# Kernel tuning notes

Measured on AMD Instinct MI355X. Metric: run time of the kernel, lower is better.

The kernel has to match this reference:

```python
import jax, jax.numpy as jnp
import numpy as np

NUM_HEADS = 16
HEAD_DIM = 80  # head_dim_ori; NPU pads 80->128 with zeros (math-neutral)


def _rotate_half(x):
    x1, x2 = jnp.split(x, 2, axis=-1)
    return jnp.concatenate([-x2, x1], axis=-1)


def setup_inputs() -> dict:
    key = jax.random.key(0)
    ks = jax.random.split(key, 7)
    S, E = 4096, 1280
    inv = jnp.asarray(1.0 / np.sqrt(E), jnp.float32)
    # rotary tables: proper cos/sin from angles for realism
    pos = jnp.arange(S, dtype=jnp.float32)[:, None]
    freqs = 1.0 / (10000.0 ** (jnp.arange(0, HEAD_DIM // 2, dtype=jnp.float32) / (HEAD_DIM // 2)))
    ang = pos * freqs[None, :]                      # [S, 40]
    ang = jnp.concatenate([ang, ang], axis=-1)      # [S, 80] rotate-half layout
    return {
        'hidden_states': jax.random.normal(ks[0], (S, E), jnp.float32),
        'cos': jnp.cos(ang),
        'sin': jnp.sin(ang),
        'w_qkv': jax.random.normal(ks[1], (3 * E, E), jnp.float32) * inv,
        'b_qkv': jax.random.normal(ks[2], (3 * E,), jnp.float32) * 0.02,
        'w_proj': jax.random.normal(ks[3], (E, E), jnp.float32) * inv,
        'b_proj': jax.random.normal(ks[4], (E,), jnp.float32) * 0.02,
    }


def reference(hidden_states, cos, sin, w_qkv, b_qkv, w_proj, b_proj):
    S, E = hidden_states.shape
    H, D = NUM_HEADS, HEAD_DIM
    # fused QKV linear (transposeB=True, hasBias=True) then split into 3
    qkv = hidden_states @ w_qkv.T + b_qkv          # [S, 3E]
    q, k, v = jnp.split(qkv, 3, axis=-1)
    q = q.reshape(S, H, D)
    k = k.reshape(S, H, D)
    v = v.reshape(S, H, D)
    # rotate-half RoPE (rotaryCoeff=2) on q and k
    c = cos[:, None, :]
    s = sin[:, None, :]
    q = q * c + _rotate_half(q) * s
    k = k * c + _rotate_half(k) * s
    # full bidirectional self-attention (PA_ENCODER), qkScale = 1/sqrt(head_dim_ori)
    scale = jnp.asarray(1.0 / np.sqrt(D), q.dtype)
    scores = jnp.einsum('shd,thd->hst', q, k) * scale   # [H, S, S]
    attn = jax.nn.softmax(scores, axis=-1)
    out = jnp.einsum('hst,thd->shd', attn, v).reshape(S, E)
    # output projection + residual add (atten_res_add)
    dense = out @ w_proj.T + b_proj
    return hidden_states + dense
```

## Files before the change

kernel.cpp:

```cpp
#include <hip/hip_runtime.h>
#include <hip/hip_bf16.h>


#define S_LEN 4096
#define E_DIM 1280
#define NH 16
#define HD 80
#define HDP 96

typedef __bf16 bf16x8 __attribute__((ext_vector_type(8)));
typedef float f32x4 __attribute__((ext_vector_type(4)));

__device__ __forceinline__ short f2bf(float x) {
    __hip_bfloat16 h = __float2bfloat16(x);
    return __builtin_bit_cast(short, h);
}
__device__ __forceinline__ float bf2f(short x) {
    return __bfloat162float(__builtin_bit_cast(__hip_bfloat16, x));
}
__device__ __forceinline__ bf16x8 ldb(const short* p) {
    return *reinterpret_cast<const bf16x8*>(p);
}
__device__ __forceinline__ unsigned cvt_pk_bf16(float a, float b) {
    unsigned r;
    asm("v_cvt_pk_bf16_f32 %0, %1, %2" : "=v"(r) : "v"(a), "v"(b));
    return r;
}
__device__ __forceinline__ void gload16(const void* g, void* l) {
    __builtin_amdgcn_global_load_lds(
        (const __attribute__((address_space(1))) unsigned int*)g,
        (__attribute__((address_space(3))) unsigned int*)l, 16, 0, 0);
}

__global__ __launch_bounds__(256) void cast3_k(const float* __restrict__ a, short* __restrict__ oa, int na4,
                                               const float* __restrict__ b, short* __restrict__ ob, int nb4,
                                               const float* __restrict__ c, short* __restrict__ oc, int nc4) {
    int j = blockIdx.x * 256 + threadIdx.x;
    const float* src;
    short* dst;
    if (j < na4) {
        src = a; dst = oa;
    } else {
        j -= na4;
        if (j < nb4) {
            src = b; dst = ob;
        } else {
            j -= nb4;
            if (j >= nc4) return;
            src = c; dst = oc;
        }
    }
    float4 v = *reinterpret_cast<const float4*>(&src[j * 4]);
    ushort4 o;
    o.x = (unsigned short)f2bf(v.x);
    o.y = (unsigned short)f2bf(v.y);
    o.z = (unsigned short)f2bf(v.z);
    o.w = (unsigned short)f2bf(v.w);
    *reinterpret_cast<ushort4*>(&dst[j * 4]) = o;
}

__global__ __launch_bounds__(512, 2) void gemm1_256_k(
    const short* __restrict__ A, const short* __restrict__ B, const float* __restrict__ bias,
    short* __restrict__ Qraw, short* __restrict__ Kraw, short* __restrict__ Vg) {
    const int K = E_DIM;
    __shared__ short As[2][2][8192];
    __shared__ short Bs[2][2][8192];
    int t = threadIdx.x;
    int lane = t & 63, w = t >> 6;
    int wr = w >> 2, wc = w & 3;
    int lr = lane & 15, lg = lane >> 4;
    int bid = blockIdx.x;
    int swz = (bid & 7) * 30 + (bid >> 3);
    int bm = swz / 15, bn = swz % 15;
    int mb = bm * 256, nb = bn * 256;

    int lgs = (t & 3) ^ ((t >> 3) & 3);
    const short* aS = A + (size_t)(mb + (t >> 2)) * K + lgs * 8;
    const short* bS = B + (size_t)(nb + (t >> 2)) * K + lgs * 8;
    const int rowStep = 128 * K;

    int aoff[2][4], boff[4];
#pragma unroll
    for (int mq = 0; mq < 2; mq++)
#pragma unroll
        for (int ii = 0; ii < 4; ii++) {
            int r = wr * 128 + mq * 64 + ii * 16 + lr;
            aoff[mq][ii] = r * 32 + ((lg ^ ((r >> 1) & 3)) * 8);
        }
#pragma unroll
    for (int n = 0; n < 4; n++) {
        int r = wc * 64 + n * 16 + lr;
        boff[n] = r * 32 + ((lg ^ ((r >> 1) & 3)) * 8);
    }

    f32x4 acc[8][4];
#pragma unroll
    for (int i = 0; i < 8; i++)
#pragma unroll
        for (int n = 0; n < 4; n++) acc[i][n] = (f32x4){0.f, 0.f, 0.f, 0.f};

#define STG_A(d, kh, kb2)                                              \
    {                                                                  \
        gload16(aS + (kb2) + (kh)*32, &As[d][kh][w * 512]);            \
        gload16(aS + rowStep + (kb2) + (kh)*32, &As[d][kh][4096 + w * 512]); \
    }
#define STG_B(d, kh, kb2)                                              \
    {                                                                  \
        gload16(bS + (kb2) + (kh)*32, &Bs[d][kh][w * 512]);            \
        gload16(bS + rowStep + (kb2) + (kh)*32, &Bs[d][kh][4096 + w * 512]); \
    }

    STG_A(0, 0, 0);
    STG_B(0, 0, 0);
    STG_A(0, 1, 0);
    STG_B(0, 1, 0);
    asm volatile("s_waitcnt vmcnt(4)" ::: "memory");
    __builtin_amdgcn_s_barrier();
    asm volatile("" ::: "memory");

    for (int kb = 0; kb < K; kb += 64) {
        int d = (kb >> 6) & 1;
        int kb2 = kb + 64;
        bool more = kb2 < K;
        bf16x8 af[4], bfr[4];

#pragma unroll
        for (int n = 0; n < 4; n++) bfr[n] = ldb(&Bs[d][0][boff[n]]);
#pragma unroll
        for (int ii = 0; ii < 4; ii++) af[ii] = ldb(&As[d][0][aoff[0][ii]]);
        if (more) STG_A(d ^ 1, 0, kb2);
        __builtin_amdgcn_s_barrier();
        asm volatile("s_waitcnt lgkmcnt(0)" ::: "memory");
        __builtin_amdgcn_sched_barrier(0);
        __builtin_amdgcn_s_setprio(1);
#pragma unroll
        for (int ii = 0; ii < 4; ii++)
#pragma unroll
            for (int n = 0; n < 4; n++)
                acc[ii][n] = __builtin_amdgcn_mfma_f32_16x16x32_bf16(af[ii], bfr[n], acc[ii][n], 0, 0, 0);
        __builtin_amdgcn_s_setprio(0);
        __builtin_amdgcn_s_barrier();
        asm volatile("" ::: "memory");

#pragma unroll
        for (int ii = 0; ii < 4; ii++) af[ii] = ldb(&As[d][0][aoff[1][ii]]);
        if (more) {
            STG_B(d ^ 1, 0, kb2);
            asm volatile("s_waitcnt vmcnt(4)" ::: "memory");
        } else {
            asm volatile("s_waitcnt vmcnt(0)" ::: "memory");
        }
        __builtin_amdgcn_s_barrier();
        asm volatile("s_waitcnt lgkmcnt(0)" ::: "memory");
        __builtin_amdgcn_sched_barrier(0);
        __builtin_amdgcn_s_setprio(1);
#pragma unroll
        for (int ii = 0; ii < 4; ii++)
#pragma unroll
            for (int n = 0; n < 4; n++)
                acc[4 + ii][n] = __builtin_amdgcn_mfma_f32_16x16x32_bf16(af[ii], bfr[n], acc[4 + ii][n], 0, 0, 0);
        __builtin_amdgcn_s_setprio(0);
        __builtin_amdgcn_s_barrier();
        asm volatile("" ::: "memory");

#pragma unroll
        for (int n = 0; n < 4; n++) bfr[n] = ldb(&Bs[d][1][boff[n]]);
#pragma unroll
        for (int ii = 0; ii < 4; ii++) af[ii] = ldb(&As[d][1][aoff[0][ii]]);
        if (more) STG_A(d ^ 1, 1, kb2);
        __builtin_amdgcn_s_barrier();
        asm volatile("s_waitcnt lgkmcnt(0)" ::: "memory");
        __builtin_amdgcn_sched_barrier(0);
        __builtin_amdgcn_s_setprio(1);
#pragma unroll
        for (int ii = 0; ii < 4; ii++)
#pragma unroll
            for (int n = 0; n < 4; n++)
                acc[ii][n] = __builtin_amdgcn_mfma_f32_16x16x32_bf16(af[ii], bfr[n], acc[ii][n], 0, 0, 0);
        __builtin_amdgcn_s_setprio(0);
        __builtin_amdgcn_s_barrier();
        asm volatile("" ::: "memory");

#pragma unroll
        for (int ii = 0; ii < 4; ii++) af[ii] = ldb(&As[d][1][aoff[1][ii]]);
        if (more) {
            STG_B(d ^ 1, 1, kb2);
            asm volatile("s_waitcnt vmcnt(4)" ::: "memory");
        }
        __builtin_amdgcn_s_barrier();
        asm volatile("s_waitcnt lgkmcnt(0)" ::: "memory");
        __builtin_amdgcn_sched_barrier(0);
        __builtin_amdgcn_s_setprio(1);
#pragma unroll
        for (int ii = 0; ii < 4; ii++)
#pragma unroll
            for (int n = 0; n < 4; n++)
                acc[4 + ii][n] = __builtin_amdgcn_mfma_f32_16x16x32_bf16(af[ii], bfr[n], acc[4 + ii][n], 0, 0, 0);
        __builtin_amdgcn_s_setprio(0);
        __builtin_amdgcn_s_barrier();
        asm volatile("" ::: "memory");
    }
#undef STG_A
#undef STG_B

    int part = nb / E_DIM;
    short* dst = (part == 0) ? Qraw : (part == 1) ? Kraw : Vg;
#pragma unroll
    for (int j = 0; j < 4; j++) {
        int n = nb + wc * 64 + j * 16 + lr;
        float bv = bias[n];
        int hd = n - part * E_DIM;
        int h = hd / HD, dd = hd - h * HD;
#pragma unroll
        for (int i = 0; i < 8; i++) {
#pragma unroll
            for (int r = 0; r < 4; r++) {
                int s = mb + wr * 128 + (i >> 2) * 64 + (i & 3) * 16 + lg * 4 + r;
                dst[(h * S_LEN + s) * HD + dd] = f2bf(acc[i][j][r] + bv);
            }
        }
    }
}

__global__ __launch_bounds__(256) void gemm_bt_k(
    const short* __restrict__ A, const short* __restrict__ B, const float* __restrict__ bias,
    const float* __restrict__ resid, float* __restrict__ Out) {
    const int K = E_DIM;
    __shared__ short As[2][128 * 64];
    __shared__ short Bs[2][128 * 64];
    int t = threadIdx.x;
    int lane = t & 63, w = t >> 6;
    int wr = w >> 1, wc = w & 1;
    int lr = lane & 15, lg = lane >> 4;
    int mb = blockIdx.y * 128, nb = blockIdx.x * 128;

    const short* asrc[4];
    const short* bsrc[4];
#pragma unroll
    for (int c = 0; c < 4; c++) {
        int p = c * 256 + t;
        int m = p >> 3;
        int kg = (p & 7) ^ (m & 7);
        asrc[c] = A + (size_t)(mb + m) * K + kg * 8;
        bsrc[c] = B + (size_t)(nb + m) * K + kg * 8;
    }
    int xa = lr & 7;
    int cx0 = ((0 * 4 + lg) ^ xa) * 8;
    int cx1 = ((1 * 4 + lg) ^ xa) * 8;
    int rowA[4], rowB[4];
#pragma unroll
    for (int i = 0; i < 4; i++) {
        rowA[i] = (wr * 64 + i * 16 + lr) * 64;
        rowB[i] = (wc * 64 + i * 16 + lr) * 64;
    }

    f32x4 acc[4][4];
#pragma unroll
    for (int i = 0; i < 4; i++)
#pragma unroll
        for (int j = 0; j < 4; j++) acc[i][j] = (f32x4){0.f, 0.f, 0.f, 0.f};

#define G_STAGE(buf, kb)                                             \
    {                                                                \
        _Pragma("unroll") for (int c = 0; c < 4; c++) {              \
            int ldso = c * 2048 + w * 512;                           \
            gload16(asrc[c] + (kb), &As[buf][ldso]);                 \
            gload16(bsrc[c] + (kb), &Bs[buf][ldso]);                 \
        }                                                            \
    }

    G_STAGE(0, 0);
    asm volatile("s_waitcnt vmcnt(0)" ::: "memory");
    __syncthreads();

    int buf = 0;
    for (int kb = 0; kb < K; kb += 64) {
        if (kb + 64 < K) G_STAGE(buf ^ 1, kb + 64);
        __builtin_amdgcn_s_setprio(1);
#pragma unroll
        for (int kk = 0; kk < 2; kk++) {
            int cx = kk ? cx1 : cx0;
            bf16x8 af[4], bfr[4];
#pragma unroll
            for (int i = 0; i < 4; i++) {
                af[i] = ldb(&As[buf][rowA[i] + cx]);
                bfr[i] = ldb(&Bs[buf][rowB[i] + cx]);
            }
#pragma unroll
            for (int i = 0; i < 4; i++)
#pragma unroll
                for (int j = 0; j < 4; j++)
                    acc[i][j] = __builtin_amdgcn_mfma_f32_16x16x32_bf16(af[i], bfr[j], acc[i][j], 0, 0, 0);
        }
        __builtin_amdgcn_s_setprio(0);
        __syncthreads();
        buf ^= 1;
    }
#undef G_STAGE

#pragma unroll
    for (int j = 0; j < 4; j++) {
        int n = nb + wc * 64 + j * 16 + lr;
        float bv = bias[n];
#pragma unroll
        for (int i = 0; i < 4; i++) {
#pragma unroll
            for (int r = 0; r < 4; r++) {
                int s = mb + wr * 64 + i * 16 + lg * 4 + r;
                Out[s * E_DIM + n] = acc[i][j][r] + bv + resid[s * E_DIM + n];
            }
        }
    }
}

__global__ __launch_bounds__(256) void rope_k(const short* __restrict__ Qraw,
                                              const short* __restrict__ Kraw,
                                              const float* __restrict__ cosp,
                                              const float* __restrict__ sinp,
                                              short* __restrict__ Qg, short* __restrict__ Kg) {
    int idx = blockIdx.x * 256 + threadIdx.x;
    int c = idx % 12;
    int sh = idx / 12;
    int s = sh & (S_LEN - 1);
    int base96 = sh * HDP + c * 8;
    if (c >= 10) {
        int4 z = {0, 0, 0, 0};
        *reinterpret_cast<int4*>(&Qg[base96]) = z;
        *reinterpret_cast<int4*>(&Kg[base96]) = z;
        return;
    }
    int d0 = c * 8;
    int dp = (d0 < 40) ? d0 + 40 : d0 - 40;
    float sgn = (d0 < 40) ? -1.f : 1.f;
    int base80 = sh * HD;
    float q[8], qp[8], k[8], kp[8], cs[8], sn[8];
    {
        int4 v;
        v = *reinterpret_cast<const int4*>(&Qraw[base80 + d0]);
        const short* sp = reinterpret_cast<const short*>(&v);
        for (int i = 0; i < 8; i++) q[i] = bf2f(sp[i]);
        v = *reinterpret_cast<const int4*>(&Qraw[base80 + dp]);
        for (int i = 0; i < 8; i++) qp[i] = bf2f(sp[i]);
        v = *reinterpret_cast<const int4*>(&Kraw[base80 + d0]);
        for (int i = 0; i < 8; i++) k[i] = bf2f(sp[i]);
        v = *reinterpret_cast<const int4*>(&Kraw[base80 + dp]);
        for (int i = 0; i < 8; i++) kp[i] = bf2f(sp[i]);
    }
    *reinterpret_cast<float4*>(&cs[0]) = *reinterpret_cast<const float4*>(&cosp[s * HD + d0]);
    *reinterpret_cast<float4*>(&cs[4]) = *reinterpret_cast<const float4*>(&cosp[s * HD + d0 + 4]);
    *reinterpret_cast<float4*>(&sn[0]) = *reinterpret_cast<const float4*>(&sinp[s * HD + d0]);
    *reinterpret_cast<float4*>(&sn[4]) = *reinterpret_cast<const float4*>(&sinp[s * HD + d0 + 4]);
    const float qscale = 0.16129849190f;
    short oq[8], ok[8];
#pragma unroll
    for (int i = 0; i < 8; i++) {
        oq[i] = f2bf((q[i] * cs[i] + sgn * qp[i] * sn[i]) * qscale);
        ok[i] = f2bf(k[i] * cs[i] + sgn * kp[i] * sn[i]);
    }
    *reinterpret_cast<int4*>(&Qg[base96]) = *reinterpret_cast<int4*>(oq);
    *reinterpret_cast<int4*>(&Kg[base96]) = *reinterpret_cast<int4*>(ok);
}

__global__ __launch_bounds__(256) void transpose_v_k(const short* __restrict__ Vg,
                                                     short* __restrict__ Vt) {
    __shared__ short tile[32][33];
    int h = blockIdx.z, sb = blockIdx.x * 32, db = blockIdx.y * 32;
    int t = threadIdx.x;
    for (int e = t; e < 1024; e += 256) {
        int si = e >> 5, dj = e & 31;
        int d = db + dj;
        tile[si][dj] = (d < HD) ? Vg[(h * S_LEN + sb + si) * HD + d] : (short)0;
    }
    __syncthreads();
    for (int e = t; e < 1024; e += 256) {
        int di = e >> 5, sj = e & 31;
        int d = db + di;
        if (d < HD) Vt[(h * HD + d) * S_LEN + sb + sj] = tile[sj][di];
    }
}

__global__ __launch_bounds__(512, 4) void attn_k(const short* __restrict__ Qg,
                                                 const short* __restrict__ Kg,
                                                 const short* __restrict__ Vt,
                                                 short* __restrict__ Ob) {
    __shared__ __align__(16) short smem[35072];
    short* ksb = smem;
    short* vsb = smem + 13312;
    short* psb = smem + 24832;

    int t = threadIdx.x;
    int lane = t & 63, w = t >> 6;
    int lr = lane & 15, lg = lane >> 4;
    int pairi = w >> 1, half = w & 1;
    int L = blockIdx.x;
    int h = ((L & 7) << 1) | (L >> 8);
    int qb = ((L >> 3) & 31) << 7;

    const short* kgp = Kg + (size_t)h * S_LEN * HDP;
    const short* vgp = Vt + (size_t)h * HD * S_LEN;

    bf16x8 qf[2][3];
#pragma unroll
    for (int qq = 0; qq < 2; qq++) {
        const short* qp = Qg + ((size_t)h * S_LEN + qb + pairi * 32 + qq * 16 + lr) * HDP;
#pragma unroll
        for (int kk = 0; kk < 3; kk++) qf[qq][kk] = ldb(qp + kk * 32 + lg * 8);
    }
    f32x4 o[2][5];
#pragma unroll
    for (int qq = 0; qq < 2; qq++)
#pragma unroll
        for (int nd = 0; nd < 5; nd++) o[qq][nd] = (f32x4){0.f, 0.f, 0.f, 0.f};
    f32x4 l4[2] = {(f32x4){0.f, 0.f, 0.f, 0.f}, (f32x4){0.f, 0.f, 0.f, 0.f}};

    int gk0 = t, rk0 = gk0 / 13, ok0 = gk0 % 13;
    if (ok0 == 12) ok0 = 0;
    const short* ksrc0 = kgp + rk0 * HDP + ok0 * 8;
    int gk1 = t + 512, rk1 = gk1 / 13, ok1 = gk1 % 13;
    if (ok1 == 12) ok1 = 0;
    const short* ksrc1 = kgp + rk1 * HDP + ok1 * 8;
    int gv0 = t, rv0 = gv0 / 9, ov0 = gv0 % 9;
    if (ov0 == 8) ov0 = 0;
    const short* vsrc0 = vgp + (size_t)rv0 * S_LEN + ov0 * 8;
    bool v1v = (t + 512) < 720;
    int gv1 = t + 512, rv1 = gv1 / 9, ov1 = gv1 % 9;
    if (ov1 == 8) ov1 = 0;
    const short* vsrc1 = vgp + (size_t)rv1 * S_LEN + ov1 * 8;

#define A_STAGE(buf, kb)                                                          \
    {                                                                             \
        gload16(ksrc0 + (size_t)(kb) * HDP, ksb + (buf)*6656 + w * 512);          \
        if (w < 5) gload16(ksrc1 + (size_t)(kb) * HDP, ksb + (buf)*6656 + 4096 + w * 512); \
        gload16(vsrc0 + (kb), vsb + (buf)*5760 + w * 512);                        \
        if (v1v) gload16(vsrc1 + (kb), vsb + (buf)*5760 + 4096 + w * 512);        \
    }

    A_STAGE(0, 0);
    asm volatile("s_waitcnt vmcnt(0)" ::: "memory");
    __syncthreads();

    short* ps = psb + w * 1280;
    int buf = 0;
    for (int kb = 0; kb < S_LEN; kb += 64) {
        if (kb + 64 < S_LEN) A_STAGE(buf ^ 1, kb + 64);
        const short* ks = ksb + buf * 6656;
        const short* vs = vsb + buf * 5760;

        f32x4 sc[2][2];
#pragma unroll
        for (int qq = 0; qq < 2; qq++)
#pragma unroll
            for (int n = 0; n < 2; n++) sc[qq][n] = (f32x4){0.f, 0.f, 0.f, 0.f};
        __builtin_amdgcn_s_setprio(1);
#pragma unroll
        for (int n = 0; n < 2; n++) {
#pragma unroll
            for (int kk = 0; kk < 3; kk++) {
                bf16x8 kf = ldb(&ks[(half * 32 + n * 16 + lr) * 104 + kk * 32 + lg * 8]);
                sc[0][n] = __builtin_amdgcn_mfma_f32_16x16x32_bf16(kf, qf[0][kk], sc[0][n], 0, 0, 0);
                sc[1][n] = __builtin_amdgcn_mfma_f32_16x16x32_bf16(kf, qf[1][kk], sc[1][n], 0, 0, 0);
            }
        }
        __builtin_amdgcn_s_setprio(0);

#pragma unroll
        for (int qq = 0; qq < 2; qq++) {
#pragma unroll
            for (int n = 0; n < 2; n++) {
#pragma unroll
                for (int r = 0; r < 4; r++) sc[qq][n][r] = __builtin_amdgcn_exp2f(sc[qq][n][r]);
                l4[qq] += sc[qq][n];
                uint2 pk;
                pk.x = cvt_pk_bf16(sc[qq][n][0], sc[qq][n][1]);
                pk.y = cvt_pk_bf16(sc[qq][n][2], sc[qq][n][3]);
                *reinterpret_cast<uint2*>(&ps[(qq * 16 + lr) * 40 + n * 16 + lg * 4]) = pk;
            }
        }

        bf16x8 pf0 = ldb(&ps[(0 * 16 + lr) * 40 + lg * 8]);
        bf16x8 pf1 = ldb(&ps[(1 * 16 + lr) * 40 + lg * 8]);
        __builtin_amdgcn_s_setprio(1);
#pragma unroll
        for (int nd = 0; nd < 5; nd++) {
            bf16x8 vf = ldb(&vs[(nd * 16 + lr) * 72 + half * 32 + lg * 8]);
            o[0][nd] = __builtin_amdgcn_mfma_f32_16x16x32_bf16(pf0, vf, o[0][nd], 0, 0, 0);
            o[1][nd] = __builtin_amdgcn_mfma_f32_16x16x32_bf16(pf1, vf, o[1][nd], 0, 0, 0);
        }
        __builtin_amdgcn_s_setprio(0);

        __syncthreads();
        buf ^= 1;
    }
#undef A_STAGE

    float lh[2];
#pragma unroll
    for (int qq = 0; qq < 2; qq++) {
        float l = l4[qq][0] + l4[qq][1] + l4[qq][2] + l4[qq][3];
        l += __shfl_xor(l, 16);
        l += __shfl_xor(l, 32);
        lh[qq] = l;
    }
    float* Osc = reinterpret_cast<float*>(smem);
    float* lsc = reinterpret_cast<float*>(smem) + 10240;
    if (half) {
#pragma unroll
        for (int qq = 0; qq < 2; qq++) {
#pragma unroll
            for (int nd = 0; nd < 5; nd++)
#pragma unroll
                for (int r = 0; r < 4; r++)
                    Osc[(pairi * 32 + qq * 16 + lg * 4 + r) * 80 + nd * 16 + lr] = o[qq][nd][r];
            if (lg == 0) lsc[pairi * 32 + qq * 16 + lr] = lh[qq];
        }
    }
    __syncthreads();
    if (!half) {
        float rl[2][4];
#pragma unroll
        for (int qq = 0; qq < 2; qq++) {
            float lt = lh[qq] + lsc[pairi * 32 + qq * 16 + lr];
#pragma unroll
            for (int r = 0; r < 4; r++) {
                float lf = __shfl(lt, lg * 4 + r);
                rl[qq][r] = __builtin_amdgcn_rcpf(lf);
            }
        }
#pragma unroll
        for (int qq = 0; qq < 2; qq++)
#pragma unroll
            for (int nd = 0; nd < 5; nd++)
#pragma unroll
                for (int r = 0; r < 4; r++) {
                    int s = qb + pairi * 32 + qq * 16 + lg * 4 + r;
                    float val = o[qq][nd][r] + Osc[(pairi * 32 + qq * 16 + lg * 4 + r) * 80 + nd * 16 + lr];
                    Ob[s * E_DIM + h * HD + nd * 16 + lr] = f2bf(val * rl[qq][r]);
                }
    }
}

extern "C" void kernel_launch(void* const* d_in, const int* in_sizes, int n_in,
                              void* d_out, int out_size, void* d_ws, size_t ws_size,
                              hipStream_t stream) {
    const float* hidden = (const float*)d_in[0];
    const float* cosp = (const float*)d_in[1];
    const float* sinp = (const float*)d_in[2];
    const float* wqkv = (const float*)d_in[3];
    const float* bqkv = (const float*)d_in[4];
    const float* wproj = (const float*)d_in[5];
    const float* bproj = (const float*)d_in[6];
    float* out = (float*)d_out;

    char* p = (char*)d_ws;
    short* Xb = (short*)p;      p += (size_t)S_LEN * E_DIM * 2;
    short* Wqkvb = (short*)p;   p += (size_t)3 * E_DIM * E_DIM * 2;
    short* Wprojb = (short*)p;  p += (size_t)E_DIM * E_DIM * 2;
    short* Qraw = (short*)p;    p += (size_t)NH * S_LEN * HD * 2;
    short* Kraw = (short*)p;    p += (size_t)NH * S_LEN * HD * 2;
    short* Vg = (short*)p;      p += (size_t)NH * S_LEN * HD * 2;
    short* Qg = (short*)p;      p += (size_t)NH * S_LEN * HDP * 2;
    short* Kg = (short*)p;      p += (size_t)NH * S_LEN * HDP * 2;
    short* Vt = (short*)p;      p += (size_t)NH * HD * S_LEN * 2;
    short* Ob = Xb;

    const int na4 = S_LEN * E_DIM / 4;
    const int nb4 = 3 * E_DIM * E_DIM / 4;
    const int nc4 = E_DIM * E_DIM / 4;
    cast3_k<<<(na4 + nb4 + nc4 + 255) / 256, 256, 0, stream>>>(
        hidden, Xb, na4, wqkv, Wqkvb, nb4, wproj, Wprojb, nc4);

    gemm1_256_k<<<dim3(240), 512, 0, stream>>>(Xb, Wqkvb, bqkv, Qraw, Kraw, Vg);

    rope_k<<<NH * S_LEN * 12 / 256, 256, 0, stream>>>(Qraw, Kraw, cosp, sinp, Qg, Kg);

    transpose_v_k<<<dim3(S_LEN / 32, 3, NH), 256, 0, stream>>>(Vg, Vt);

    attn_k<<<dim3(512), 512, 0, stream>>>(Qg, Kg, Vt, Ob);

    gemm_bt_k<<<dim3(E_DIM / 128, S_LEN / 128), 256, 0, stream>>>(
        Ob, Wprojb, bproj, hidden, out);
}
```

Before: 206.5 us.

## Keep P in registers for PV MFMA and store QKV row-major

After: 197.3 us. 4.4% less time.

```diff
diff --git a/kernel.cpp b/kernel.cpp
--- a/kernel.cpp
+++ b/kernel.cpp
@@ -205,18 +205,18 @@
 
     int part = nb / E_DIM;
     short* dst = (part == 0) ? Qraw : (part == 1) ? Kraw : Vg;
+    int nloc = nb - part * E_DIM;
 #pragma unroll
     for (int j = 0; j < 4; j++) {
-        int n = nb + wc * 64 + j * 16 + lr;
-        float bv = bias[n];
-        int hd = n - part * E_DIM;
-        int h = hd / HD, dd = hd - h * HD;
+        int cn = wc * 64 + j * 16 + lr;
+        float bv = bias[nb + cn];
+        int col = nloc + cn;
 #pragma unroll
         for (int i = 0; i < 8; i++) {
 #pragma unroll
             for (int r = 0; r < 4; r++) {
                 int s = mb + wr * 128 + (i >> 2) * 64 + (i & 3) * 16 + lg * 4 + r;
-                dst[(h * S_LEN + s) * HD + dd] = f2bf(acc[i][j][r] + bv);
+                dst[(size_t)s * E_DIM + col] = f2bf(acc[i][j][r] + bv);
             }
         }
     }
@@ -320,9 +320,9 @@
                                               short* __restrict__ Qg, short* __restrict__ Kg) {
     int idx = blockIdx.x * 256 + threadIdx.x;
     int c = idx % 12;
-    int sh = idx / 12;
-    int s = sh & (S_LEN - 1);
-    int base96 = sh * HDP + c * 8;
+    int hh = (idx / 12) & 15;
+    int s = idx / 192;
+    int base96 = ((hh * S_LEN + s)) * HDP + c * 8;
     if (c >= 10) {
         int4 z = {0, 0, 0, 0};
         *reinterpret_cast<int4*>(&Qg[base96]) = z;
@@ -332,7 +332,7 @@
     int d0 = c * 8;
     int dp = (d0 < 40) ? d0 + 40 : d0 - 40;
     float sgn = (d0 < 40) ? -1.f : 1.f;
-    int base80 = sh * HD;
+    int base80 = s * E_DIM + hh * HD;
     float q[8], qp[8], k[8], kp[8], cs[8], sn[8];
     {
         int4 v;
@@ -369,13 +369,14 @@
     for (int e = t; e < 1024; e += 256) {
         int si = e >> 5, dj = e & 31;
         int d = db + dj;
-        tile[si][dj] = (d < HD) ? Vg[(h * S_LEN + sb + si) * HD + d] : (short)0;
+        tile[si][dj] = (d < HD) ? Vg[(size_t)(sb + si) * E_DIM + h * HD + d] : (short)0;
     }
     __syncthreads();
     for (int e = t; e < 1024; e += 256) {
         int di = e >> 5, sj = e & 31;
         int d = db + di;
-        if (d < HD) Vt[(h * HD + d) * S_LEN + sb + sj] = tile[sj][di];
+        int pj = ((sj >> 2) & 3) * 8 + ((sj >> 4) & 1) * 4 + (sj & 3);
+        if (d < HD) Vt[(h * HD + d) * S_LEN + sb + pj] = tile[sj][di];
     }
 }
 
@@ -383,10 +384,9 @@
                                                  const short* __restrict__ Kg,
                                                  const short* __restrict__ Vt,
                                                  short* __restrict__ Ob) {
-    __shared__ __align__(16) short smem[35072];
+    __shared__ __align__(16) short smem[24832];
     short* ksb = smem;
     short* vsb = smem + 13312;
-    short* psb = smem + 24832;
 
     int t = threadIdx.x;
     int lane = t & 63, w = t >> 6;
@@ -439,7 +439,6 @@
     asm volatile("s_waitcnt vmcnt(0)" ::: "memory");
     __syncthreads();
 
-    short* ps = psb + w * 1280;
     int buf = 0;
     for (int kb = 0; kb < S_LEN; kb += 64) {
         if (kb + 64 < S_LEN) A_STAGE(buf ^ 1, kb + 64);
@@ -463,6 +462,7 @@
         }
         __builtin_amdgcn_s_setprio(0);
 
+        bf16x8 pa[2];
 #pragma unroll
         for (int qq = 0; qq < 2; qq++) {
 #pragma unroll
@@ -470,21 +470,21 @@
 #pragma unroll
                 for (int r = 0; r < 4; r++) sc[qq][n][r] = __builtin_amdgcn_exp2f(sc[qq][n][r]);
                 l4[qq] += sc[qq][n];
-                uint2 pk;
-                pk.x = cvt_pk_bf16(sc[qq][n][0], sc[qq][n][1]);
-                pk.y = cvt_pk_bf16(sc[qq][n][2], sc[qq][n][3]);
-                *reinterpret_cast<uint2*>(&ps[(qq * 16 + lr) * 40 + n * 16 + lg * 4]) = pk;
             }
-        }
-
-        bf16x8 pf0 = ldb(&ps[(0 * 16 + lr) * 40 + lg * 8]);
-        bf16x8 pf1 = ldb(&ps[(1 * 16 + lr) * 40 + lg * 8]);
+            uint4 pw;
+            pw.x = cvt_pk_bf16(sc[qq][0][0], sc[qq][0][1]);
+            pw.y = cvt_pk_bf16(sc[qq][0][2], sc[qq][0][3]);
+            pw.z = cvt_pk_bf16(sc[qq][1][0], sc[qq][1][1]);
+            pw.w = cvt_pk_bf16(sc[qq][1][2], sc[qq][1][3]);
+            pa[qq] = __builtin_bit_cast(bf16x8, pw);
+        }
+
         __builtin_amdgcn_s_setprio(1);
 #pragma unroll
         for (int nd = 0; nd < 5; nd++) {
             bf16x8 vf = ldb(&vs[(nd * 16 + lr) * 72 + half * 32 + lg * 8]);
-            o[0][nd] = __builtin_amdgcn_mfma_f32_16x16x32_bf16(pf0, vf, o[0][nd], 0, 0, 0);
-            o[1][nd] = __builtin_amdgcn_mfma_f32_16x16x32_bf16(pf1, vf, o[1][nd], 0, 0, 0);
+            o[0][nd] = __builtin_amdgcn_mfma_f32_16x16x32_bf16(pa[0], vf, o[0][nd], 0, 0, 0);
+            o[1][nd] = __builtin_amdgcn_mfma_f32_16x16x32_bf16(pa[1], vf, o[1][nd], 0, 0, 0);
         }
         __builtin_amdgcn_s_setprio(0);
 
@@ -555,9 +555,9 @@
     short* Xb = (short*)p;      p += (size_t)S_LEN * E_DIM * 2;
     short* Wqkvb = (short*)p;   p += (size_t)3 * E_DIM * E_DIM * 2;
     short* Wprojb = (short*)p;  p += (size_t)E_DIM * E_DIM * 2;
-    short* Qraw = (short*)p;    p += (size_t)NH * S_LEN * HD * 2;
-    short* Kraw = (short*)p;    p += (size_t)NH * S_LEN * HD * 2;
-    short* Vg = (short*)p;      p += (size_t)NH * S_LEN * HD * 2;
+    short* Qraw = (short*)p;    p += (size_t)S_LEN * E_DIM * 2;
+    short* Kraw = (short*)p;    p += (size_t)S_LEN * E_DIM * 2;
+    short* Vg = (short*)p;      p += (size_t)S_LEN * E_DIM * 2;
     short* Qg = (short*)p;      p += (size_t)NH * S_LEN * HDP * 2;
     short* Kg = (short*)p;      p += (size_t)NH * S_LEN * HDP * 2;
     short* Vt = (short*)p;      p += (size_t)NH * HD * S_LEN * 2;
@@ -571,7 +571,7 @@
 
     gemm1_256_k<<<dim3(240), 512, 0, stream>>>(Xb, Wqkvb, bqkv, Qraw, Kraw, Vg);
 
-    rope_k<<<NH * S_LEN * 12 / 256, 256, 0, stream>>>(Qraw, Kraw, cosp, sinp, Qg, Kg);
+    rope_k<<<S_LEN * 192 / 256, 256, 0, stream>>>(Qraw, Kraw, cosp, sinp, Qg, Kg);
 
     transpose_v_k<<<dim3(S_LEN / 32, 3, NH), 256, 0, stream>>>(Vg, Vt);
 
```
